# Kernel optimization log

Hardware: AMD Instinct MI355X
Metric: run time of the kernel (lower is better)

## Reference

```python
import jax, jax.numpy as jnp
import numpy as np

N = 8192       # nodes per graph
E = 262144     # edges per graph (avg degree 32)
H = 8          # attention heads
C = 128        # hidden dim per head (H*C = 1024 to match Linear(1024,128))
IN = 128       # input feature dim
NEG_SLOPE = 0.2


def _gat_conv(x, edge_index, W, att_src, att_dst, bias):
    """PyG GATConv (concat=True, add_self_loops=True, shared lin for src/dst)."""
    n = x.shape[0]
    loop = jnp.arange(n, dtype=edge_index.dtype)
    src = jnp.concatenate([edge_index[0], loop])  # [E+N]
    dst = jnp.concatenate([edge_index[1], loop])
    h = (x @ W).reshape(n, H, C)                         # [N,H,C]
    a_src = jnp.sum(h * att_src, axis=-1)                # [N,H]
    a_dst = jnp.sum(h * att_dst, axis=-1)                # [N,H]
    e = jax.nn.leaky_relu(a_src[src] + a_dst[dst], NEG_SLOPE)   # [E+N,H]
    m = jax.ops.segment_max(e, dst, num_segments=n)      # per-dst max for stability
    ex = jnp.exp(e - m[dst])
    den = jax.ops.segment_sum(ex, dst, num_segments=n)
    alpha = ex / den[dst]                                # [E+N,H] neighborhood softmax
    out = jax.ops.segment_sum(h[src] * alpha[:, :, None], dst, num_segments=n)
    return out.reshape(n, H * C) + bias                  # [N, H*C]


def setup_inputs() -> dict:
    key = jax.random.key(0)
    ks = jax.random.split(key, 12)
    s = 0.05  # keep activations in a sane range
    return {
        "x1": jax.random.normal(ks[0], (N, IN), jnp.float32),
        "edge_index1": jax.random.randint(ks[1], (2, E), 0, N, dtype=jnp.int64),
        "W1": jax.random.normal(ks[2], (IN, H * C), jnp.float32) * s,
        "att_src1": jax.random.normal(ks[3], (H, C), jnp.float32) * s,
        "att_dst1": jax.random.normal(ks[4], (H, C), jnp.float32) * s,
        "b1": jnp.zeros((H * C,), jnp.float32),
        "x2": jax.random.normal(ks[5], (N, IN), jnp.float32),
        "edge_index2": jax.random.randint(ks[6], (2, E), 0, N, dtype=jnp.int64),
        "W2": jax.random.normal(ks[7], (IN, H * C), jnp.float32) * s,
        "att_src2": jax.random.normal(ks[8], (H, C), jnp.float32) * s,
        "att_dst2": jax.random.normal(ks[9], (H, C), jnp.float32) * s,
        "b2": jnp.zeros((H * C,), jnp.float32),
        "Wl": jax.random.normal(ks[10], (H * C, 128), jnp.float32) * s,
        "bl": jnp.zeros((128,), jnp.float32),
    }


def reference(x1, edge_index1, W1, att_src1, att_dst1, b1,
              x2, edge_index2, W2, att_src2, att_dst2, b2, Wl, bl):
    emb1 = _gat_conv(x1, edge_index1, W1, att_src1, att_dst1, b1)  # [N1,1024]
    emb2 = _gat_conv(x2, edge_index2, W2, att_src2, att_dst2, b2)  # [N2,1024]
    scores = emb1 @ emb2.T                                          # [N1,N2]
    w1 = jax.nn.softmax(scores, axis=1)
    w2 = jax.nn.softmax(scores, axis=0)
    cross1 = (w2 @ emb2) @ Wl + bl      # [N1,128]
    cross2 = (w1.T @ emb1) @ Wl + bl    # [N2,128]
    return (jnp.mean(cross1, axis=0), jnp.mean(cross2, axis=0))
```

## Files before the change

kernel.cpp:

```cpp
#include <hip/hip_runtime.h>


#define NN 8192
#define EE 262144
#define NEG 0.2f

#define BKT 128
#define RNG (NN / BKT)
#define CAP 2560
#define CHK (EE / 128)

#define U_CNT   0
#define U_GACC  (U_CNT + 4*BKT)
#define U_ZEND  (U_GACC + 2048)
#define U_U     (U_ZEND)
#define U_ASRC  (U_U + 2*2048)
#define U_ADST  (U_ASRC + 2*NN*8)
#define U_PR    (U_ADST + 2*NN*8)
#define U_BIND  (U_PR + 2*NN*16)
#define U_BINS  (U_BIND + 2*BKT*CAP)
#define ZERO_BYTES ((size_t)U_ZEND * 4)

__global__ __launch_bounds__(512) void k_bin(
    const int* __restrict__ ei1, const int* __restrict__ ei2,
    const float* __restrict__ W1, const float* __restrict__ as1,
    const float* __restrict__ ad1,
    const float* __restrict__ W2, const float* __restrict__ as2,
    const float* __restrict__ ad2,
    int* __restrict__ cnt, int* __restrict__ binD, int* __restrict__ binS,
    float* __restrict__ u) {
  int g = blockIdx.y;
  int t = threadIdx.x;
  if (blockIdx.x >= 128) {
    int sd = blockIdx.x - 128;
    const float* Wg = g ? W2 : W1;
    const float* att = g ? (sd ? ad2 : as2) : (sd ? ad1 : as1);
    float* uo = u + g * 2048 + sd * 1024;
    for (int o = t; o < 1024; o += 512) {
      int head = o >> 7, k = o & 127;
      const float4* wr = (const float4*)(Wg + (size_t)k * 1024 + head * 128);
      const float4* ar = (const float4*)(att + head * 128);
      float s = 0.f;
#pragma unroll 8
      for (int c = 0; c < 32; ++c) {
        float4 w4 = wr[c], a4 = ar[c];
        s += w4.x * a4.x + w4.y * a4.y + w4.z * a4.z + w4.w * a4.w;
      }
      uo[o] = s;
    }
    return;
  }
  const int* ei = g ? ei2 : ei1;
  __shared__ int hD[BKT], hS[BKT], bD[BKT], bS[BKT], cD[BKT], cS[BKT];
  for (int i = t; i < BKT; i += 512) { hD[i] = 0; hS[i] = 0; cD[i] = 0; cS[i] = 0; }
  __syncthreads();
  int e0 = blockIdx.x * CHK;
  for (int i = t; i < CHK; i += 512) {
    int s = ei[e0 + i], d = ei[EE + e0 + i];
    atomicAdd(&hD[d >> 6], 1);
    atomicAdd(&hS[s >> 6], 1);
  }
  __syncthreads();
  for (int i = t; i < BKT; i += 512) {
    bD[i] = atomicAdd(cnt + (2 * g + 0) * BKT + i, hD[i]);
    bS[i] = atomicAdd(cnt + (2 * g + 1) * BKT + i, hS[i]);
  }
  __syncthreads();
  int* bdg = binD + (size_t)g * BKT * CAP;
  int* bsg = binS + (size_t)g * BKT * CAP;
  for (int i = t; i < CHK; i += 512) {
    int s = ei[e0 + i], d = ei[EE + e0 + i];
    int kb = d >> 6;
    int p = bD[kb] + atomicAdd(&cD[kb], 1);
    bdg[kb * CAP + p] = (s << 6) | (d & 63);
    kb = s >> 6;
    p = bS[kb] + atomicAdd(&cS[kb], 1);
    bsg[kb * CAP + p] = (d << 6) | (s & 63);
  }
}

__global__ __launch_bounds__(512) void k_a(
    const float* __restrict__ x1, const float* __restrict__ x2,
    const float* __restrict__ u,
    float* __restrict__ asrc, float* __restrict__ adst) {
  int gph = blockIdx.y, cb = blockIdx.x;
  __shared__ float xs[64][129];
  __shared__ float us[16][128];
  int t = threadIdx.x;
  const float* ug = u + gph * 2048;
  for (int i = t; i < 2048; i += 512) us[i >> 7][i & 127] = ug[i];
  const float* x = gph ? x2 : x1;
  const int n0 = cb * 64;
  const float4* xb4 = (const float4*)(x + (size_t)n0 * 128);
  for (int i = t; i < 64 * 32; i += 512) {
    float4 v = xb4[i];
    int r = i >> 5, c = (i & 31) * 4;
    xs[r][c] = v.x; xs[r][c + 1] = v.y; xs[r][c + 2] = v.z; xs[r][c + 3] = v.w;
  }
  __syncthreads();
  int nl = t & 63;
  int j0 = (t >> 6) * 2;
  float a0 = 0.f, a1 = 0.f;
#pragma unroll 4
  for (int k = 0; k < 128; ++k) {
    float xv = xs[nl][k];
    a0 += xv * us[j0 + 0][k];
    a1 += xv * us[j0 + 1][k];
  }
  int n = n0 + nl;
  float* outp = (j0 < 8) ? (asrc + gph * (NN * 8) + n * 8 + j0)
                         : (adst + gph * (NN * 8) + n * 8 + (j0 - 8));
  outp[0] = a0; outp[1] = a1;
}

__global__ __launch_bounds__(512) void k_den(
    const int* __restrict__ cnt, const int* __restrict__ binD,
    const float* __restrict__ asrc, const float* __restrict__ adst,
    float* __restrict__ pr) {
  int gph = blockIdx.y, b = blockIdx.x;
  int lo = b * RNG;
  const float* as = asrc + gph * (NN * 8);
  const float* ad = adst + gph * (NN * 8);
  float2* prg = (float2*)pr + (size_t)gph * (NN * 8);
  __shared__ float den[RNG * 8];
  __shared__ float ads[RNG * 8];
  int t = threadIdx.x;
  for (int i = t; i < RNG * 8; i += 512) {
    float avv = ad[lo * 8 + i];
    float v = as[lo * 8 + i] + avv;
    v = v > 0.f ? v : NEG * v;
    ads[i] = avv;
    den[i] = __expf(v);
  }
  __syncthreads();
  int n = cnt[(2 * gph + 0) * BKT + b];
  const int* recs = binD + (size_t)gph * BKT * CAP + b * CAP;
  int rid = t >> 3, h = t & 7;
  for (int base = 0; base < n; base += 256) {
    int rv[4]; bool ok[4]; float sv[4];
#pragma unroll
    for (int uu = 0; uu < 4; ++uu) {
      int i = base + uu * 64 + rid;
      ok[uu] = i < n;
      rv[uu] = ok[uu] ? recs[i] : 0;
    }
#pragma unroll
    for (int uu = 0; uu < 4; ++uu)
      sv[uu] = ok[uu] ? as[(rv[uu] >> 6) * 8 + h] : 0.f;
#pragma unroll
    for (int uu = 0; uu < 4; ++uu) {
      if (ok[uu]) {
        int dl = rv[uu] & 63;
        float v = sv[uu] + ads[dl * 8 + h];
        v = v > 0.f ? v : NEG * v;
        atomicAdd(&den[dl * 8 + h], __expf(v));
      }
    }
  }
  __syncthreads();
  for (int i = t; i < RNG * 8; i += 512)
    prg[lo * 8 + i] = make_float2(ads[i], 1.0f / den[i]);
}

__global__ __launch_bounds__(512) void k_waccG(
    const int* __restrict__ cnt, const int* __restrict__ binS,
    const float* __restrict__ asrc, const float* __restrict__ pr,
    const float* __restrict__ x1, const float* __restrict__ x2,
    float* __restrict__ gacc) {
  int gph = blockIdx.y, b = blockIdx.x;
  int lo = b * RNG;
  const float* as = asrc + gph * (NN * 8);
  const float2* prg = (const float2*)pr + (size_t)gph * (NN * 8);
  __shared__ float wv[RNG * 8];
  __shared__ float asx[RNG * 8];
  int t = threadIdx.x;
  for (int i = t; i < RNG * 8; i += 512) {
    float sva = as[lo * 8 + i];
    float2 f2 = prg[lo * 8 + i];
    float v = sva + f2.x;
    v = v > 0.f ? v : NEG * v;
    asx[i] = sva;
    wv[i] = __expf(v) * f2.y;
  }
  __syncthreads();
  int n = cnt[(2 * gph + 1) * BKT + b];
  const int* recs = binS + (size_t)gph * BKT * CAP + b * CAP;
  int rid = t >> 3, h = t & 7;
  for (int base = 0; base < n; base += 256) {
    int rv[4]; bool ok[4]; float2 pv[4];
#pragma unroll
    for (int uu = 0; uu < 4; ++uu) {
      int i = base + uu * 64 + rid;
      ok[uu] = i < n;
      rv[uu] = ok[uu] ? recs[i] : 0;
    }
#pragma unroll
    for (int uu = 0; uu < 4; ++uu)
      pv[uu] = ok[uu] ? prg[(size_t)(rv[uu] >> 6) * 8 + h] : make_float2(0.f, 0.f);
#pragma unroll
    for (int uu = 0; uu < 4; ++uu) {
      if (ok[uu]) {
        int sl = rv[uu] & 63;
        float v = asx[sl * 8 + h] + pv[uu].x;
        v = v > 0.f ? v : NEG * v;
        atomicAdd(&wv[sl * 8 + h], __expf(v) * pv[uu].y);
      }
    }
  }
  __syncthreads();
  const float* x = gph ? x2 : x1;
  float* gg = gacc + gph * 1024;
  int k = t & 127;
  int h0 = (t >> 7) * 2;
  int n0 = b * RNG;
  float a0 = 0.f, a1 = 0.f;
#pragma unroll 4
  for (int nl = 0; nl < RNG; ++nl) {
    float xv = x[(size_t)(n0 + nl) * 128 + k];
    a0 += xv * wv[nl * 8 + h0];
    a1 += xv * wv[nl * 8 + h0 + 1];
  }
  atomicAdd(gg + (h0 + 0) * 128 + k, a0);
  atomicAdd(gg + (h0 + 1) * 128 + k, a1);
}

__global__ __launch_bounds__(512) void k_tail(
    const float* __restrict__ gacc,
    const float* __restrict__ W1, const float* __restrict__ b1,
    const float* __restrict__ W2, const float* __restrict__ b2,
    const float* __restrict__ Wl, const float* __restrict__ bl,
    float* __restrict__ out) {
  __shared__ float gld[2][1024];
  __shared__ float memb[2][1024];
  __shared__ float po[512];
  int t = threadIdx.x;
  for (int i = t; i < 2048; i += 512) gld[i >> 10][i & 1023] = gacc[i];
  __syncthreads();
  for (int o = t; o < 2048; o += 512) {
    int g2 = o >> 10, e = o & 1023;
    const float* W = g2 ? W2 : W1;
    const float* bb = g2 ? b2 : b1;
    const float* gr = &gld[g2][(e >> 7) * 128];
    float s = 0.f;
#pragma unroll 8
    for (int k = 0; k < 128; ++k) s += gr[k] * W[(size_t)k * 1024 + e];
    memb[g2][e] = s * (1.0f / (float)NN) + bb[e];
  }
  __syncthreads();
  {
    int o = t & 255;
    int kh = t >> 8;
    int j = o & 127;
    const float* m = (o < 128) ? memb[1] : memb[0];
    float s = 0.f;
#pragma unroll 8
    for (int k = kh * 512; k < kh * 512 + 512; ++k)
      s += m[k] * Wl[(size_t)k * 128 + j];
    po[t] = s;
    __syncthreads();
    if (t < 256) out[t] = po[t] + po[t + 256] + bl[t & 127];
  }
}

extern "C" void kernel_launch(void* const* d_in, const int* in_sizes, int n_in,
                              void* d_out, int out_size, void* d_ws, size_t ws_size,
                              hipStream_t stream) {
  const float* x1  = (const float*)d_in[0];
  const int*   ei1 = (const int*)d_in[1];
  const float* W1  = (const float*)d_in[2];
  const float* as1 = (const float*)d_in[3];
  const float* ad1 = (const float*)d_in[4];
  const float* b1  = (const float*)d_in[5];
  const float* x2  = (const float*)d_in[6];
  const int*   ei2 = (const int*)d_in[7];
  const float* W2  = (const float*)d_in[8];
  const float* as2 = (const float*)d_in[9];
  const float* ad2 = (const float*)d_in[10];
  const float* b2  = (const float*)d_in[11];
  const float* Wl  = (const float*)d_in[12];
  const float* bl  = (const float*)d_in[13];
  float* out = (float*)d_out;

  int*   cnt  = (int*)d_ws + U_CNT;
  float* gacc = (float*)d_ws + U_GACC;
  float* u    = (float*)d_ws + U_U;
  float* asrc = (float*)d_ws + U_ASRC;
  float* adst = (float*)d_ws + U_ADST;
  float* pr   = (float*)d_ws + U_PR;
  int*   binD = (int*)d_ws + U_BIND;
  int*   binS = (int*)d_ws + U_BINS;

  hipMemsetAsync(d_ws, 0, ZERO_BYTES, stream);

  k_bin<<<dim3(130, 2), 512, 0, stream>>>(ei1, ei2, W1, as1, ad1,
                                          W2, as2, ad2, cnt, binD, binS, u);
  k_a<<<dim3(128, 2), 512, 0, stream>>>(x1, x2, u, asrc, adst);
  k_den<<<dim3(BKT, 2), 512, 0, stream>>>(cnt, binD, asrc, adst, pr);
  k_waccG<<<dim3(BKT, 2), 512, 0, stream>>>(cnt, binS, asrc, pr, x1, x2, gacc);
  k_tail<<<1, 512, 0, stream>>>(gacc, W1, b1, W2, b2, Wl, bl, out);
}
```

Baseline: 219.2 us.

## Fuse attention-coefficient projection into binning kernel and split tail across two blocks

Merges the k_a kernel into the binning kernel. Extra blocks now each recompute the W·att vectors into shared memory and then project their 64-node slice to asrc/adst, which removes one launch and the global round-trip through u. The tail kernel is split into two blocks, one per output graph, with the Wl reduction divided four ways. The cost is redundant W·att computation in each of the 256 extra blocks, which reads the full W matrix per block.

```diff
diff --git a/kernel.cpp b/kernel.cpp
--- a/kernel.cpp
+++ b/kernel.cpp
@@ -13,57 +13,92 @@
 #define U_CNT   0
 #define U_GACC  (U_CNT + 4*BKT)
 #define U_ZEND  (U_GACC + 2048)
-#define U_U     (U_ZEND)
-#define U_ASRC  (U_U + 2*2048)
+#define U_ASRC  (U_ZEND)
 #define U_ADST  (U_ASRC + 2*NN*8)
 #define U_PR    (U_ADST + 2*NN*8)
 #define U_BIND  (U_PR + 2*NN*16)
 #define U_BINS  (U_BIND + 2*BKT*CAP)
 #define ZERO_BYTES ((size_t)U_ZEND * 4)
 
-__global__ __launch_bounds__(512) void k_bin(
+union SMemBA {
+  struct { int hD[BKT]; int hS[BKT]; int bD[BKT]; int bS[BKT]; int cD[BKT]; int cS[BKT]; } bin;
+  struct { float xs[64][129]; float us[16][128]; } a;
+};
+
+__global__ __launch_bounds__(512) void k_binA(
     const int* __restrict__ ei1, const int* __restrict__ ei2,
-    const float* __restrict__ W1, const float* __restrict__ as1,
-    const float* __restrict__ ad1,
-    const float* __restrict__ W2, const float* __restrict__ as2,
-    const float* __restrict__ ad2,
+    const float* __restrict__ x1, const float* __restrict__ W1,
+    const float* __restrict__ as1, const float* __restrict__ ad1,
+    const float* __restrict__ x2, const float* __restrict__ W2,
+    const float* __restrict__ as2, const float* __restrict__ ad2,
     int* __restrict__ cnt, int* __restrict__ binD, int* __restrict__ binS,
-    float* __restrict__ u) {
+    float* __restrict__ asrc, float* __restrict__ adst) {
+  __shared__ SMemBA sm;
   int g = blockIdx.y;
   int t = threadIdx.x;
+
   if (blockIdx.x >= 128) {
-    int sd = blockIdx.x - 128;
+    int cb = blockIdx.x - 128;
     const float* Wg = g ? W2 : W1;
-    const float* att = g ? (sd ? ad2 : as2) : (sd ? ad1 : as1);
-    float* uo = u + g * 2048 + sd * 1024;
+    const float* ats = g ? as2 : as1;
+    const float* atd = g ? ad2 : ad1;
     for (int o = t; o < 1024; o += 512) {
       int head = o >> 7, k = o & 127;
       const float4* wr = (const float4*)(Wg + (size_t)k * 1024 + head * 128);
-      const float4* ar = (const float4*)(att + head * 128);
-      float s = 0.f;
+      const float4* asr = (const float4*)(ats + head * 128);
+      const float4* adr = (const float4*)(atd + head * 128);
+      float ss = 0.f, dd = 0.f;
 #pragma unroll 8
       for (int c = 0; c < 32; ++c) {
-        float4 w4 = wr[c], a4 = ar[c];
-        s += w4.x * a4.x + w4.y * a4.y + w4.z * a4.z + w4.w * a4.w;
+        float4 w4 = wr[c];
+        float4 a4 = asr[c], b4 = adr[c];
+        ss += w4.x * a4.x + w4.y * a4.y + w4.z * a4.z + w4.w * a4.w;
+        dd += w4.x * b4.x + w4.y * b4.y + w4.z * b4.z + w4.w * b4.w;
       }
-      uo[o] = s;
-    }
+      sm.a.us[head][k] = ss;
+      sm.a.us[8 + head][k] = dd;
+    }
+    const float* x = g ? x2 : x1;
+    const int n0 = cb * 64;
+    const float4* xb4 = (const float4*)(x + (size_t)n0 * 128);
+    for (int i = t; i < 64 * 32; i += 512) {
+      float4 v = xb4[i];
+      int r = i >> 5, c = (i & 31) * 4;
+      sm.a.xs[r][c] = v.x; sm.a.xs[r][c + 1] = v.y;
+      sm.a.xs[r][c + 2] = v.z; sm.a.xs[r][c + 3] = v.w;
+    }
+    __syncthreads();
+    int nl = t & 63;
+    int j0 = (t >> 6) * 2;
+    float a0 = 0.f, a1 = 0.f;
+#pragma unroll 4
+    for (int k = 0; k < 128; ++k) {
+      float xv = sm.a.xs[nl][k];
+      a0 += xv * sm.a.us[j0 + 0][k];
+      a1 += xv * sm.a.us[j0 + 1][k];
+    }
+    int n = n0 + nl;
+    float* outp = (j0 < 8) ? (asrc + g * (NN * 8) + n * 8 + j0)
+                           : (adst + g * (NN * 8) + n * 8 + (j0 - 8));
+    outp[0] = a0; outp[1] = a1;
     return;
   }
+
   const int* ei = g ? ei2 : ei1;
-  __shared__ int hD[BKT], hS[BKT], bD[BKT], bS[BKT], cD[BKT], cS[BKT];
-  for (int i = t; i < BKT; i += 512) { hD[i] = 0; hS[i] = 0; cD[i] = 0; cS[i] = 0; }
+  for (int i = t; i < BKT; i += 512) {
+    sm.bin.hD[i] = 0; sm.bin.hS[i] = 0; sm.bin.cD[i] = 0; sm.bin.cS[i] = 0;
+  }
   __syncthreads();
   int e0 = blockIdx.x * CHK;
   for (int i = t; i < CHK; i += 512) {
     int s = ei[e0 + i], d = ei[EE + e0 + i];
-    atomicAdd(&hD[d >> 6], 1);
-    atomicAdd(&hS[s >> 6], 1);
+    atomicAdd(&sm.bin.hD[d >> 6], 1);
+    atomicAdd(&sm.bin.hS[s >> 6], 1);
   }
   __syncthreads();
   for (int i = t; i < BKT; i += 512) {
-    bD[i] = atomicAdd(cnt + (2 * g + 0) * BKT + i, hD[i]);
-    bS[i] = atomicAdd(cnt + (2 * g + 1) * BKT + i, hS[i]);
+    sm.bin.bD[i] = atomicAdd(cnt + (2 * g + 0) * BKT + i, sm.bin.hD[i]);
+    sm.bin.bS[i] = atomicAdd(cnt + (2 * g + 1) * BKT + i, sm.bin.hS[i]);
   }
   __syncthreads();
   int* bdg = binD + (size_t)g * BKT * CAP;
@@ -71,46 +106,12 @@
   for (int i = t; i < CHK; i += 512) {
     int s = ei[e0 + i], d = ei[EE + e0 + i];
     int kb = d >> 6;
-    int p = bD[kb] + atomicAdd(&cD[kb], 1);
+    int p = sm.bin.bD[kb] + atomicAdd(&sm.bin.cD[kb], 1);
     bdg[kb * CAP + p] = (s << 6) | (d & 63);
     kb = s >> 6;
-    p = bS[kb] + atomicAdd(&cS[kb], 1);
+    p = sm.bin.bS[kb] + atomicAdd(&sm.bin.cS[kb], 1);
     bsg[kb * CAP + p] = (d << 6) | (s & 63);
   }
-}
-
-__global__ __launch_bounds__(512) void k_a(
-    const float* __restrict__ x1, const float* __restrict__ x2,
-    const float* __restrict__ u,
-    float* __restrict__ asrc, float* __restrict__ adst) {
-  int gph = blockIdx.y, cb = blockIdx.x;
-  __shared__ float xs[64][129];
-  __shared__ float us[16][128];
-  int t = threadIdx.x;
-  const float* ug = u + gph * 2048;
-  for (int i = t; i < 2048; i += 512) us[i >> 7][i & 127] = ug[i];
-  const float* x = gph ? x2 : x1;
-  const int n0 = cb * 64;
-  const float4* xb4 = (const float4*)(x + (size_t)n0 * 128);
-  for (int i = t; i < 64 * 32; i += 512) {
-    float4 v = xb4[i];
-    int r = i >> 5, c = (i & 31) * 4;
-    xs[r][c] = v.x; xs[r][c + 1] = v.y; xs[r][c + 2] = v.z; xs[r][c + 3] = v.w;
-  }
-  __syncthreads();
-  int nl = t & 63;
-  int j0 = (t >> 6) * 2;
-  float a0 = 0.f, a1 = 0.f;
-#pragma unroll 4
-  for (int k = 0; k < 128; ++k) {
-    float xv = xs[nl][k];
-    a0 += xv * us[j0 + 0][k];
-    a1 += xv * us[j0 + 1][k];
-  }
-  int n = n0 + nl;
-  float* outp = (j0 < 8) ? (asrc + gph * (NN * 8) + n * 8 + j0)
-                         : (adst + gph * (NN * 8) + n * 8 + (j0 - 8));
-  outp[0] = a0; outp[1] = a1;
 }
 
 __global__ __launch_bounds__(512) void k_den(
@@ -224,41 +225,40 @@
   atomicAdd(gg + (h0 + 1) * 128 + k, a1);
 }
 
-__global__ __launch_bounds__(512) void k_tail(
+__global__ __launch_bounds__(512) void k_mo(
     const float* __restrict__ gacc,
     const float* __restrict__ W1, const float* __restrict__ b1,
     const float* __restrict__ W2, const float* __restrict__ b2,
     const float* __restrict__ Wl, const float* __restrict__ bl,
     float* __restrict__ out) {
-  __shared__ float gld[2][1024];
-  __shared__ float memb[2][1024];
+  __shared__ float gl[1024];
+  __shared__ float membL[1024];
   __shared__ float po[512];
+  int b = blockIdx.x;
+  int gsel = 1 - b;
+  const float* W = gsel ? W2 : W1;
+  const float* bb = gsel ? b2 : b1;
   int t = threadIdx.x;
-  for (int i = t; i < 2048; i += 512) gld[i >> 10][i & 1023] = gacc[i];
-  __syncthreads();
-  for (int o = t; o < 2048; o += 512) {
-    int g2 = o >> 10, e = o & 1023;
-    const float* W = g2 ? W2 : W1;
-    const float* bb = g2 ? b2 : b1;
-    const float* gr = &gld[g2][(e >> 7) * 128];
+  for (int i = t; i < 1024; i += 512) gl[i] = gacc[gsel * 1024 + i];
+  __syncthreads();
+  for (int o = t; o < 1024; o += 512) {
+    const float* gr = &gl[(o >> 7) * 128];
     float s = 0.f;
 #pragma unroll 8
-    for (int k = 0; k < 128; ++k) s += gr[k] * W[(size_t)k * 1024 + e];
-    memb[g2][e] = s * (1.0f / (float)NN) + bb[e];
+    for (int k = 0; k < 128; ++k) s += gr[k] * W[(size_t)k * 1024 + o];
+    membL[o] = s * (1.0f / (float)NN) + bb[o];
   }
   __syncthreads();
   {
-    int o = t & 255;
-    int kh = t >> 8;
-    int j = o & 127;
-    const float* m = (o < 128) ? memb[1] : memb[0];
+    int j = t & 127, kc = t >> 7;
     float s = 0.f;
 #pragma unroll 8
-    for (int k = kh * 512; k < kh * 512 + 512; ++k)
-      s += m[k] * Wl[(size_t)k * 128 + j];
+    for (int k = kc * 256; k < kc * 256 + 256; ++k)
+      s += membL[k] * Wl[(size_t)k * 128 + j];
     po[t] = s;
     __syncthreads();
-    if (t < 256) out[t] = po[t] + po[t + 256] + bl[t & 127];
+    if (t < 128)
+      out[b * 128 + t] = po[t] + po[t + 128] + po[t + 256] + po[t + 384] + bl[t];
   }
 }
 
@@ -283,7 +283,6 @@
 
   int*   cnt  = (int*)d_ws + U_CNT;
   float* gacc = (float*)d_ws + U_GACC;
-  float* u    = (float*)d_ws + U_U;
   float* asrc = (float*)d_ws + U_ASRC;
   float* adst = (float*)d_ws + U_ADST;
   float* pr   = (float*)d_ws + U_PR;
@@ -292,10 +291,10 @@
 
   hipMemsetAsync(d_ws, 0, ZERO_BYTES, stream);
 
-  k_bin<<<dim3(130, 2), 512, 0, stream>>>(ei1, ei2, W1, as1, ad1,
-                                          W2, as2, ad2, cnt, binD, binS, u);
-  k_a<<<dim3(128, 2), 512, 0, stream>>>(x1, x2, u, asrc, adst);
+  k_binA<<<dim3(256, 2), 512, 0, stream>>>(ei1, ei2, x1, W1, as1, ad1,
+                                           x2, W2, as2, ad2,
+                                           cnt, binD, binS, asrc, adst);
   k_den<<<dim3(BKT, 2), 512, 0, stream>>>(cnt, binD, asrc, adst, pr);
   k_waccG<<<dim3(BKT, 2), 512, 0, stream>>>(cnt, binS, asrc, pr, x1, x2, gacc);
-  k_tail<<<1, 512, 0, stream>>>(gacc, W1, b1, W2, b2, Wl, bl, out);
-}
+  k_mo<<<2, 512, 0, stream>>>(gacc, W1, b1, W2, b2, Wl, bl, out);
+}
```

Result: no change. 218.5 us (-0.3%).
